# Kernel optimization log

Hardware: AMD Instinct MI355X
Metric: run time of the kernel (lower is better)

Reference implementation:

```python
import jax, jax.numpy as jnp
import numpy as np

B, ZP, ZR, H, MEL, CH, RHY, T = 64, 128, 128, 2048, 130, 12, 3, 32


def _gru(x, h, wih, whh, bih, bhh):
    # torch.nn.GRUCell semantics, gate order (r, z, n)
    gi = x @ wih.T + bih
    gh = h @ whh.T + bhh
    ir, iz, inn = jnp.split(gi, 3, axis=-1)
    hr, hz, hn = jnp.split(gh, 3, axis=-1)
    r = jax.nn.sigmoid(ir + hr)
    u = jax.nn.sigmoid(iz + hz)
    n = jnp.tanh(inn + r * hn)
    return (1.0 - u) * n + u * h


def setup_inputs() -> dict:
    key = jax.random.key(0)
    ks = jax.random.split(key, 13)
    s = 0.02
    rn = lambda k, shp: jax.random.normal(k, shp, dtype=jnp.float32) * s
    return {
        'z1': jax.random.normal(ks[0], (B, ZP), dtype=jnp.float32),
        'z2': jax.random.normal(ks[1], (B, ZR), dtype=jnp.float32),
        'condition': jax.random.uniform(ks[2], (B, T, CH), dtype=jnp.float32),
        'w_ih0': rn(ks[3], (3 * H, ZR + RHY)), 'w_hh0': rn(ks[4], (3 * H, H)),
        'b_ih0': jnp.zeros((3 * H,), jnp.float32), 'b_hh0': jnp.zeros((3 * H,), jnp.float32),
        'w_ih1': rn(ks[5], (3 * H, ZP + MEL + RHY + CH)), 'w_hh1': rn(ks[6], (3 * H, H)),
        'b_ih1': jnp.zeros((3 * H,), jnp.float32), 'b_hh1': jnp.zeros((3 * H,), jnp.float32),
        'w_ih2': rn(ks[7], (3 * H, H)), 'w_hh2': rn(ks[8], (3 * H, H)),
        'b_ih2': jnp.zeros((3 * H,), jnp.float32), 'b_hh2': jnp.zeros((3 * H,), jnp.float32),
        'wi0': rn(ks[9], (H, ZR)), 'bi0': jnp.zeros((H,), jnp.float32),
        'wo0': rn(ks[10], (RHY, H)), 'bo0': jnp.zeros((RHY,), jnp.float32),
        'wi1': rn(ks[11], (H, ZP)), 'bi1': jnp.zeros((H,), jnp.float32),
        'wo1': rn(ks[12], (MEL, H)), 'bo1': jnp.zeros((MEL,), jnp.float32),
    }


def _forward(z1, z2, condition, w_ih0, w_hh0, b_ih0, b_hh0, w_ih1, w_hh1, b_ih1,
             b_hh1, w_ih2, w_hh2, b_ih2, b_hh2, wi0, bi0, wo0, bo0, wi1, bi1, wo1, bo1):
    b = z1.shape[0]

    # --- rhythm decoder (teacher_force=False: argmax one-hot feedback) ---
    def rhy_step(carry, _):
        out, hx = carry
        hx = _gru(jnp.concatenate([out, z2], axis=1), hx, w_ih0, w_hh0, b_ih0, b_hh0)
        lo = jax.nn.log_softmax(hx @ wo0.T + bo0, axis=-1)  # [b, RHY]
        out = jax.nn.one_hot(jnp.argmax(lo, axis=1), RHY, dtype=lo.dtype)
        return (out, hx), lo

    out0 = jnp.zeros((b, RHY), jnp.float32).at[:, -1].set(1.0)
    h0 = jnp.tanh(z2 @ wi0.T + bi0)
    _, rhy = jax.lax.scan(rhy_step, (out0, h0), None, length=T)  # [T, b, RHY]

    # --- final (melody) decoder ---
    def fin_step(carry, xt):
        out, ha, hb = carry
        r_t, c_t, i = xt
        inp = jnp.concatenate([out, r_t, z1, c_t], axis=1)  # [b, MEL+RHY+ZP+CH]
        ha = _gru(inp, ha, w_ih1, w_hh1, b_ih1, b_hh1)
        hb = _gru(ha, jnp.where(i == 0, ha, hb), w_ih2, w_hh2, b_ih2, b_hh2)
        lo = jax.nn.log_softmax(hb @ wo1.T + bo1, axis=-1)  # [b, MEL]
        out = jax.nn.one_hot(jnp.argmax(lo, axis=1), MEL, dtype=lo.dtype)
        return (out, ha, hb), lo

    outm = jnp.zeros((b, MEL), jnp.float32).at[:, -1].set(1.0)
    h1 = jnp.tanh(z1 @ wi1.T + bi1)
    cond_t = jnp.transpose(condition, (1, 0, 2))  # [T, b, CH]
    _, mel = jax.lax.scan(fin_step, (outm, h1, jnp.zeros_like(h1)),
                          (rhy, cond_t, jnp.arange(T)))
    return jnp.transpose(mel, (1, 0, 2))  # [b, T, MEL]


def reference(z1, z2, condition, w_ih0, w_hh0, b_ih0, b_hh0, w_ih1, w_hh1, b_ih1,
              b_hh1, w_ih2, w_hh2, b_ih2, b_hh2, wi0, bi0, wo0, bo0, wi1, bi1, wo1, bo1):
    return _forward(z1, z2, condition, w_ih0, w_hh0, b_ih0, b_hh0, w_ih1, w_hh1,
                    b_ih1, b_hh1, w_ih2, w_hh2, b_ih2, b_hh2, wi0, bi0, wo0, bo0,
                    wi1, bi1, wo1, bo1)
```

## Files before the change

### kernel.cpp

```cpp
#include <hip/hip_runtime.h>
#include <hip/hip_bf16.h>
#include <math.h>

#define Bsz  64
#define Hd   2048
#define G3   6144
#define MELn 130
#define CHn  12
#define RHYn 3
#define Tn   32

__device__ __forceinline__ float sigf(float x) { return 1.0f / (1.0f + expf(-x)); }

__global__ void prep_misc(const float* __restrict__ z1, const float* __restrict__ z2,
                          const float* __restrict__ cond,
                          float* __restrict__ z1t, float* __restrict__ z2t,
                          float* __restrict__ cond_t, int* __restrict__ rhy_idx,
                          int* __restrict__ mel_idx, int* __restrict__ cnts)
{
    int idx = blockIdx.x * 256 + threadIdx.x;
    if (idx < 128 * Bsz) {
        int j = idx >> 6, b = idx & 63;
        z1t[idx] = z1[b * 128 + j];
        z2t[idx] = z2[b * 128 + j];
    }
    if (idx < Tn * CHn * Bsz) {
        int t = idx / (CHn * Bsz);
        int r = idx - t * CHn * Bsz;
        int j = r >> 6, b = r & 63;
        cond_t[idx] = cond[b * (Tn * CHn) + t * CHn + j];
    }
    if (idx < Bsz) { rhy_idx[idx] = RHYn - 1; mel_idx[idx] = MELn - 1; }
    if (idx < 4) cnts[idx] = 0;
}

__global__ __launch_bounds__(256) void init_h_k(
    const float* __restrict__ z1t, const float* __restrict__ z2t,
    const float* __restrict__ wi0, const float* __restrict__ bi0,
    const float* __restrict__ wi1, const float* __restrict__ bi1,
    float* __restrict__ h0_out, float* __restrict__ h1_out)
{
    int lane = threadIdx.x & 63, wave = threadIdx.x >> 6;
    int j = blockIdx.x * 4 + wave;
    int which = blockIdx.y;
    const float* zt = which ? z1t : z2t;
    const float* wi = which ? wi1 : wi0;
    const float* bi = which ? bi1 : bi0;
    float* outh = which ? h1_out : h0_out;
    const float4* w4 = (const float4*)(wi + (size_t)j * 128);
    float acc = 0.f;
#pragma unroll 8
    for (int i = 0; i < 32; i++) {
        float4 w = w4[i];
        int k = i * 4;
        acc = fmaf(zt[(k + 0) * 64 + lane], w.x, acc);
        acc = fmaf(zt[(k + 1) * 64 + lane], w.y, acc);
        acc = fmaf(zt[(k + 2) * 64 + lane], w.z, acc);
        acc = fmaf(zt[(k + 3) * 64 + lane], w.w, acc);
    }
    outh[j * 64 + lane] = tanhf(acc + bi[j]);
}

__global__ __launch_bounds__(256) void gi_const_k(
    const float* __restrict__ z1t, const float* __restrict__ z2t,
    const float* __restrict__ w_ih0, const float* __restrict__ b_ih0,
    const float* __restrict__ w_ih1, const float* __restrict__ b_ih1,
    float* __restrict__ gi0c, float* __restrict__ gi1c)
{
    int lane = threadIdx.x & 63, wave = threadIdx.x >> 6;
    int row = blockIdx.x * 4 + wave;
    int which = blockIdx.y;
    const float* zt; const float* w; float acc; float* dst;
    if (which == 0) { zt = z2t; w = w_ih0 + (size_t)row * 131 + RHYn;          acc = b_ih0[row]; dst = gi0c; }
    else            { zt = z1t; w = w_ih1 + (size_t)row * 273 + (MELn + RHYn); acc = b_ih1[row]; dst = gi1c; }
#pragma unroll 4
    for (int i = 0; i < 128; i++) acc = fmaf(zt[i * 64 + lane], w[i], acc);
    dst[(size_t)row * 64 + lane] = acc;
}

__device__ __forceinline__ void transpose_body(
    const float* __restrict__ in, float* __restrict__ out, int R, int C, int Rout,
    int bx, int by, float* tile)
{
    int c0 = bx * 64, r0 = by * 64;
    int t = threadIdx.x;
    int cl = t & 63, rw = t >> 6;
#pragma unroll
    for (int i = 0; i < 16; ++i) {
        int rl = rw + i * 4;
        int r = r0 + rl, c = c0 + cl;
        float v = (r < R && c < C) ? in[(size_t)r * C + c] : 0.f;
        tile[rl * 65 + cl] = v;
    }
    __syncthreads();
#pragma unroll
    for (int i = 0; i < 16; ++i) {
        int c_loc = rw + i * 4;
        int r_loc = cl;
        int oc = c0 + c_loc, orow = r0 + r_loc;
        if (oc < C && orow < R)
            out[(size_t)oc * Rout + orow] = tile[r_loc * 65 + c_loc];
    }
}

__global__ __launch_bounds__(256) void transpose4_k(
    const float* __restrict__ a, const float* __restrict__ b,
    const float* __restrict__ c, const float* __restrict__ d,
    float* __restrict__ oa, float* __restrict__ ob,
    float* __restrict__ oc, float* __restrict__ od)
{
    __shared__ float tile[64 * 65];
    const float* in; float* out;
    switch (blockIdx.z) {
        case 0: in = a; out = oa; break;
        case 1: in = b; out = ob; break;
        case 2: in = c; out = oc; break;
        default: in = d; out = od; break;
    }
    transpose_body(in, out, G3, Hd, G3, blockIdx.x, blockIdx.y, tile);
}

__global__ __launch_bounds__(256) void transpose1_k(
    const float* __restrict__ in, float* __restrict__ out, int R, int C, int Rout)
{
    __shared__ float tile[64 * 65];
    transpose_body(in, out, R, C, Rout, blockIdx.x, blockIdx.y, tile);
}

__device__ __forceinline__ void mm8_body(
    const float* __restrict__ WT, const float* __restrict__ x,
    float* __restrict__ part, int tile, int slot, float* xs)
{
    int tid = threadIdx.x;
    int rg = tid & 15, bg = tid >> 4;
    int r0 = tile * 128 + rg * 8;
    int b0 = bg * 4;

    float acc[8][4];
#pragma unroll
    for (int i = 0; i < 8; i++)
#pragma unroll
        for (int j = 0; j < 4; j++) acc[i][j] = 0.f;

    for (int ph = 0; ph < 2; ++ph) {
        int kp = slot * 256 + ph * 128;
        __syncthreads();
        {
            const float4* src = (const float4*)(x + (size_t)kp * 64);
            float4* dst = (float4*)xs;
#pragma unroll
            for (int i = 0; i < 8; i++) dst[tid + i * 256] = src[tid + i * 256];
        }
        __syncthreads();
        const float* wp = WT + (size_t)kp * G3 + r0;
#pragma unroll 4
        for (int k = 0; k < 128; ++k) {
            float4 xv = *(const float4*)&xs[k * 64 + b0];
            float w[8];
            *(float4*)&w[0] = *(const float4*)wp;
            *(float4*)&w[4] = *(const float4*)(wp + 4);
            wp += G3;
#pragma unroll
            for (int i = 0; i < 8; i++) {
                acc[i][0] = fmaf(w[i], xv.x, acc[i][0]);
                acc[i][1] = fmaf(w[i], xv.y, acc[i][1]);
                acc[i][2] = fmaf(w[i], xv.z, acc[i][2]);
                acc[i][3] = fmaf(w[i], xv.w, acc[i][3]);
            }
        }
    }

    size_t base = (size_t)slot * 393216 + b0;
    int prow0 = tile * 128 + rg * 8;
#pragma unroll
    for (int i = 0; i < 8; i++)
        *(float4*)&part[base + (size_t)(prow0 + i) * 64] = *(float4*)acc[i];
}

__global__ __launch_bounds__(256) void fusedA_k(
    const float* __restrict__ WT0h, const float* __restrict__ hr, float* __restrict__ partR,
    const float* __restrict__ wo0, const float* __restrict__ bo0,
    float* __restrict__ rlo_prev, int* __restrict__ rhy_idx,
    const float* __restrict__ WT1h, const float* __restrict__ ha, float* __restrict__ partM,
    const float* __restrict__ WTo1, const float* __restrict__ hbPrev,
    float* __restrict__ lpart, const float* __restrict__ bo1,
    float* __restrict__ outp, int tout, int* __restrict__ mel_idx,
    int* __restrict__ cnt, int flags)
{
    __shared__ float smem[8192];
    int flat = blockIdx.x, tid = threadIdx.x;

    if (flat == 0) {
        if (!(flags & 2)) return;
        int lane = tid & 63, wv = tid >> 6;
        const float* hc = hr + wv * 512 * 64;
        const float* w0 = wo0 + wv * 512;
        const float* w1 = wo0 + Hd + wv * 512;
        const float* w2 = wo0 + 2 * Hd + wv * 512;
        float a0 = 0.f, a1 = 0.f, a2 = 0.f;
#pragma unroll 4
        for (int k = 0; k < 512; k++) {
            float hv = hc[k * 64 + lane];
            a0 = fmaf(hv, w0[k], a0);
            a1 = fmaf(hv, w1[k], a1);
            a2 = fmaf(hv, w2[k], a2);
        }
        smem[(0 * 4 + wv) * 64 + lane] = a0;
        smem[(1 * 4 + wv) * 64 + lane] = a1;
        smem[(2 * 4 + wv) * 64 + lane] = a2;
        __syncthreads();
        if (wv == 0) {
            float l0 = smem[0 * 64 + lane] + smem[1 * 64 + lane] + smem[2 * 64 + lane] + smem[3 * 64 + lane] + bo0[0];
            float l1 = smem[4 * 64 + lane] + smem[5 * 64 + lane] + smem[6 * 64 + lane] + smem[7 * 64 + lane] + bo0[1];
            float l2 = smem[8 * 64 + lane] + smem[9 * 64 + lane] + smem[10 * 64 + lane] + smem[11 * 64 + lane] + bo0[2];
            int am; float mx;
            if (l0 >= l1 && l0 >= l2) { am = 0; mx = l0; }
            else if (l1 >= l2)        { am = 1; mx = l1; }
            else                      { am = 2; mx = l2; }
            float s = expf(l0 - mx) + expf(l1 - mx) + expf(l2 - mx);
            float ls = logf(s);
            rlo_prev[lane * 3 + 0] = l0 - mx - ls;
            rlo_prev[lane * 3 + 1] = l1 - mx - ls;
            rlo_prev[lane * 3 + 2] = l2 - mx - ls;
            rhy_idx[lane] = am;
        }
        return;
    }

    if (flat <= 16) {
        if (!(flags & 8)) return;
        int li = flat - 1;
        int ltile = li & 1, lslot = li >> 1;
        int rg = tid & 15, bg = tid >> 4;
        int r0 = ltile * 128 + rg * 8;
        int b0 = bg * 4;
        int k0 = lslot * 256;

        float acc[8][4];
#pragma unroll
        for (int i = 0; i < 8; i++)
#pragma unroll
            for (int j = 0; j < 4; j++) acc[i][j] = 0.f;

        bool fast = (r0 + 7 < MELn);
        for (int ph = 0; ph < 2; ++ph) {
            int kp = k0 + ph * 128;
            __syncthreads();
            {
                const float4* src = (const float4*)(hbPrev + (size_t)kp * 64);
                float4* dst = (float4*)smem;
#pragma unroll
                for (int i = 0; i < 8; i++) dst[tid + i * 256] = src[tid + i * 256];
            }
            __syncthreads();
            if (fast) {
                const float* wp = WTo1 + (size_t)kp * 132 + r0;
#pragma unroll 4
                for (int k = 0; k < 128; ++k) {
                    float4 xv = *(const float4*)&smem[k * 64 + b0];
                    float w[8];
                    *(float4*)&w[0] = *(const float4*)wp;
                    *(float4*)&w[4] = *(const float4*)(wp + 4);
                    wp += 132;
#pragma unroll
                    for (int i = 0; i < 8; i++) {
                        acc[i][0] = fmaf(w[i], xv.x, acc[i][0]);
                        acc[i][1] = fmaf(w[i], xv.y, acc[i][1]);
                        acc[i][2] = fmaf(w[i], xv.z, acc[i][2]);
                        acc[i][3] = fmaf(w[i], xv.w, acc[i][3]);
                    }
                }
            } else {
                for (int k = 0; k < 128; ++k) {
                    float4 xv = *(const float4*)&smem[k * 64 + b0];
                    const float* wrow = WTo1 + (size_t)(k0 + ph * 128 + k) * 132;
                    float w[8];
#pragma unroll
                    for (int i = 0; i < 8; i++) {
                        int rc = r0 + i; if (rc > MELn - 1) rc = MELn - 1;
                        w[i] = wrow[rc];
                    }
#pragma unroll
                    for (int i = 0; i < 8; i++) {
                        acc[i][0] = fmaf(w[i], xv.x, acc[i][0]);
                        acc[i][1] = fmaf(w[i], xv.y, acc[i][1]);
                        acc[i][2] = fmaf(w[i], xv.z, acc[i][2]);
                        acc[i][3] = fmaf(w[i], xv.w, acc[i][3]);
                    }
                }
            }
        }
        size_t base = (size_t)lslot * 8320 + b0;
#pragma unroll
        for (int i = 0; i < 8; i++) {
            int prow = ltile * 128 + rg * 8 + i;
            int pc = prow < MELn ? prow : (MELn - 1);
            *(float4*)&lpart[base + (size_t)pc * 64] = *(float4*)acc[i];
        }

        __shared__ int lastf;
        __threadfence();
        __syncthreads();
        if (tid == 0) lastf = (atomicAdd(cnt, 1) == 15);
        __syncthreads();
        if (!lastf) return;
        __threadfence();

        int b = tid & 63, q = tid >> 6;
        int rLo = q * 33, rHi = rLo + 33; if (rHi > MELn) rHi = MELn;
        float mx = -1e30f; int am = MELn;
        for (int r = rLo; r < rHi; r++) {
            float v = bo1[r];
#pragma unroll
            for (int s = 0; s < 8; s++) v += lpart[s * 8320 + r * 64 + b];
            lpart[r * 64 + b] = v;
            if (v > mx) { mx = v; am = r; }
        }
        float* qmax = smem;
        int*   qam  = (int*)(smem + 256);
        float* qsum = smem + 512;
        qmax[q * 64 + b] = mx; qam[q * 64 + b] = am;
        __syncthreads();
        float gm = qmax[b]; int ga = qam[b];
#pragma unroll
        for (int qq = 1; qq < 4; qq++) {
            float v = qmax[qq * 64 + b];
            if (v > gm) { gm = v; ga = qam[qq * 64 + b]; }
        }
        float ps = 0.f;
        for (int r = rLo; r < rHi; r++) ps += expf(lpart[r * 64 + b] - gm);
        qsum[q * 64 + b] = ps;
        __syncthreads();
        float ls = logf(qsum[b] + qsum[64 + b] + qsum[128 + b] + qsum[192 + b]);
        if (tid < 64) mel_idx[b] = ga;
        for (int r = rLo; r < rHi; r++)
            outp[(size_t)b * Tn * MELn + tout * MELn + r] = lpart[r * 64 + b] - gm - ls;
        __syncthreads();
        if (tid == 0) *cnt = 0;
        return;
    }

    if (flat < 401) {
        if (!(flags & 1)) return;
        int e = flat - 17;
        mm8_body(WT0h, hr, partR, e % 48, e / 48, smem);
        return;
    }
    {
        if (!(flags & 4)) return;
        int e = flat - 401;
        mm8_body(WT1h, ha, partM, e % 48, e / 48, smem);
    }
}

__global__ __launch_bounds__(256) void fusedB_k(
    const float* __restrict__ partR, const float* __restrict__ gi0c,
    const float* __restrict__ w_ih0, const float* __restrict__ b_hh0,
    const float* __restrict__ hr_in, float* __restrict__ hr_out,
    const int* __restrict__ rhy_idx,
    const float* __restrict__ partM, const float* __restrict__ gi1c,
    const float* __restrict__ w_ih1, const float* __restrict__ b_hh1,
    const float* __restrict__ ha_in, float* __restrict__ ha_out,
    const int* __restrict__ mel_idx, const float* __restrict__ rlo,
    const float* __restrict__ cdt, int flags)
{
    __shared__ float red[48 * 68];
    int flat = blockIdx.x, tid = threadIdx.x;
    int wv = tid >> 6, lane = tid & 63;
    int jj = lane >> 4, bq = lane & 15;
    int isMel = (flat >= 512);
    if (isMel) { if (!(flags & 2)) return; }
    else       { if (!(flags & 1)) return; }
    int jbase = (isMel ? flat - 512 : flat) * 4;
    const float* part = isMel ? partM : partR;

    float s0[4], s1[4], s2[4];
#pragma unroll
    for (int q = 0; q < 4; q++) { s0[q] = 0.f; s1[q] = 0.f; s2[q] = 0.f; }
#pragma unroll
    for (int ss = 0; ss < 2; ss++) {
        const float* p = part + (size_t)(wv * 2 + ss) * 393216
                       + (size_t)(jbase + jj) * 64 + bq * 4;
        float4 v0 = *(const float4*)(p);
        float4 v1 = *(const float4*)(p + 2048 * 64);
        float4 v2 = *(const float4*)(p + 4096 * 64);
        s0[0] += v0.x; s0[1] += v0.y; s0[2] += v0.z; s0[3] += v0.w;
        s1[0] += v1.x; s1[1] += v1.y; s1[2] += v1.z; s1[3] += v1.w;
        s2[0] += v2.x; s2[1] += v2.y; s2[2] += v2.z; s2[3] += v2.w;
    }
    int rbase = (wv * 4 + jj) * 3;
    *(float4*)&red[(rbase + 0) * 68 + bq * 4] = make_float4(s0[0], s0[1], s0[2], s0[3]);
    *(float4*)&red[(rbase + 1) * 68 + bq * 4] = make_float4(s1[0], s1[1], s1[2], s1[3]);
    *(float4*)&red[(rbase + 2) * 68 + bq * 4] = make_float4(s2[0], s2[1], s2[2], s2[3]);
    __syncthreads();

    int b = lane, jw = wv;
    int j = jbase + jw;
    float ar = 0.f, az = 0.f, an = 0.f;
#pragma unroll
    for (int ww = 0; ww < 4; ww++) {
        int rb = (ww * 4 + jw) * 3;
        ar += red[(rb + 0) * 68 + b];
        az += red[(rb + 1) * 68 + b];
        an += red[(rb + 2) * 68 + b];
    }

    if (!isMel) {
        int oi = rhy_idx[b];
        float gir = gi0c[j * 64 + b]            + w_ih0[(size_t)j * 131 + oi];
        float giz = gi0c[(j + 2048) * 64 + b]   + w_ih0[(size_t)(j + 2048) * 131 + oi];
        float gin = gi0c[(j + 4096) * 64 + b]   + w_ih0[(size_t)(j + 4096) * 131 + oi];
        float rg = sigf(gir + ar + b_hh0[j]);
        float ug = sigf(giz + az + b_hh0[j + 2048]);
        float ng = tanhf(gin + rg * (an + b_hh0[j + 4096]));
        float hp = hr_in[j * 64 + b];
        hr_out[j * 64 + b] = (1.f - ug) * ng + ug * hp;
    } else {
        int oi = mel_idx[b];
        float r0 = rlo[b * 3 + 0], r1 = rlo[b * 3 + 1], r2 = rlo[b * 3 + 2];
        float cd[12];
#pragma unroll
        for (int q = 0; q < 12; q++) cd[q] = cdt[q * 64 + b];
        float gi[3];
#pragma unroll
        for (int g = 0; g < 3; g++) {
            int row = j + g * 2048;
            const float* wrow = w_ih1 + (size_t)row * 273;
            float v = gi1c[row * 64 + b] + wrow[oi];
            v = fmaf(r0, wrow[130], v);
            v = fmaf(r1, wrow[131], v);
            v = fmaf(r2, wrow[132], v);
#pragma unroll
            for (int q = 0; q < 12; q++) v = fmaf(cd[q], wrow[261 + q], v);
            gi[g] = v;
        }
        float rg = sigf(gi[0] + ar + b_hh1[j]);
        float ug = sigf(gi[1] + az + b_hh1[j + 2048]);
        float ng = tanhf(gi[2] + rg * (an + b_hh1[j + 4096]));
        float hp = ha_in[j * 64 + b];
        ha_out[j * 64 + b] = (1.f - ug) * ng + ug * hp;
    }
}

__global__ __launch_bounds__(256) void mmg2_k(
    const float* __restrict__ WTa, const float* __restrict__ xa,
    const float* __restrict__ WTb, const float* __restrict__ xb,
    float* __restrict__ part)
{
    __shared__ float xs[128 * 64];
    int tid = threadIdx.x;
    int tile = blockIdx.x, slot = blockIdx.y;
    const float* WT; const float* x; int tLoc;
    if (tile < 48) { WT = WTa; x = xa; tLoc = tile; }
    else           { WT = WTb; x = xb; tLoc = tile - 48; }
    int rg = tid & 15, bg = tid >> 4;
    int r0 = tLoc * 128 + rg * 8;
    int b0 = bg * 4;
    int k0 = slot * 512;

    float acc[8][4];
#pragma unroll
    for (int i = 0; i < 8; i++)
#pragma unroll
        for (int j = 0; j < 4; j++) acc[i][j] = 0.f;

    for (int ph = 0; ph < 4; ++ph) {
        int kp = k0 + ph * 128;
        __syncthreads();
        {
            const float4* src = (const float4*)(x + (size_t)kp * 64);
            float4* dst = (float4*)xs;
#pragma unroll
            for (int i = 0; i < 8; i++) dst[tid + i * 256] = src[tid + i * 256];
        }
        __syncthreads();
        const float* wp = WT + (size_t)kp * G3 + r0;
#pragma unroll 4
        for (int k = 0; k < 128; ++k) {
            float4 xv = *(const float4*)&xs[k * 64 + b0];
            float w[8];
            *(float4*)&w[0] = *(const float4*)wp;
            *(float4*)&w[4] = *(const float4*)(wp + 4);
            wp += G3;
#pragma unroll
            for (int i = 0; i < 8; i++) {
                acc[i][0] = fmaf(w[i], xv.x, acc[i][0]);
                acc[i][1] = fmaf(w[i], xv.y, acc[i][1]);
                acc[i][2] = fmaf(w[i], xv.z, acc[i][2]);
                acc[i][3] = fmaf(w[i], xv.w, acc[i][3]);
            }
        }
    }

    size_t base = (size_t)slot * 786432 + b0;
    int prow0 = tile * 128 + rg * 8;
#pragma unroll
    for (int i = 0; i < 8; i++)
        *(float4*)&part[base + (size_t)(prow0 + i) * 64] = *(float4*)acc[i];
}

__global__ __launch_bounds__(256) void mel2_epi(
    const float* __restrict__ part, const float* __restrict__ b_ih,
    const float* __restrict__ b_hh, const float* __restrict__ hb_in,
    float* __restrict__ hb_out)
{
    __shared__ float red[96 * 68];
    int tid = threadIdx.x;
    int wv = tid >> 6, lane = tid & 63;
    int jj = lane >> 4, bq = lane & 15;
    int jbase = blockIdx.x * 4;

    float s[6][4];
    {
        const float* p = part + (size_t)wv * 786432
                       + (size_t)(jbase + jj) * 64 + bq * 4;
#pragma unroll
        for (int g = 0; g < 6; g++) {
            float4 v = *(const float4*)(p + (size_t)g * 2048 * 64);
            s[g][0] = v.x; s[g][1] = v.y; s[g][2] = v.z; s[g][3] = v.w;
        }
    }
    int rbase = (wv * 4 + jj) * 6;
#pragma unroll
    for (int g = 0; g < 6; g++)
        *(float4*)&red[(rbase + g) * 68 + bq * 4] = make_float4(s[g][0], s[g][1], s[g][2], s[g][3]);
    __syncthreads();

    int b = lane, jw = wv;
    int j = jbase + jw;
    float air = 0.f, aiz = 0.f, ain = 0.f, ahr = 0.f, ahz = 0.f, ahn = 0.f;
#pragma unroll
    for (int ww = 0; ww < 4; ww++) {
        int rb = (ww * 4 + jw) * 6;
        air += red[(rb + 0) * 68 + b];
        aiz += red[(rb + 1) * 68 + b];
        ain += red[(rb + 2) * 68 + b];
        ahr += red[(rb + 3) * 68 + b];
        ahz += red[(rb + 4) * 68 + b];
        ahn += red[(rb + 5) * 68 + b];
    }
    float rg = sigf(air + b_ih[j] + ahr + b_hh[j]);
    float ug = sigf(aiz + b_ih[j + 2048] + ahz + b_hh[j + 2048]);
    float ng = tanhf(ain + b_ih[j + 4096] + rg * (ahn + b_hh[j + 4096]));
    float hp = hb_in[j * 64 + b];
    hb_out[j * 64 + b] = (1.f - ug) * ng + ug * hp;
}

__global__ __launch_bounds__(256) void mm2_k(
    const float* __restrict__ WTa, const float* __restrict__ xa,
    const float* __restrict__ WTb, const float* __restrict__ xb,
    float* __restrict__ part, int splitTile, int kc, int nrows, int wstride,
    int partStride)
{
    __shared__ float xs[128 * 64];
    int tid = threadIdx.x;
    int tile = blockIdx.x, slot = blockIdx.y;
    const float* WT; const float* x; int tLoc;
    if (tile < splitTile) { WT = WTa; x = xa; tLoc = tile; }
    else                  { WT = WTb; x = xb; tLoc = tile - splitTile; }
    int rg = tid & 15, bg = tid >> 4;
    int r0 = tLoc * 128 + rg * 8;
    int b0 = bg * 4;
    int k0 = slot * kc;

    float acc[8][4];
#pragma unroll
    for (int i = 0; i < 8; i++)
#pragma unroll
        for (int j = 0; j < 4; j++) acc[i][j] = 0.f;

    bool fast = (r0 + 7 < nrows);
    int nPhase = kc >> 7;
    for (int ph = 0; ph < nPhase; ++ph) {
        int kp = k0 + ph * 128;
        __syncthreads();
        {
            const float4* src = (const float4*)(x + (size_t)kp * 64);
            float4* dst = (float4*)xs;
#pragma unroll
            for (int i = 0; i < 8; i++) dst[tid + i * 256] = src[tid + i * 256];
        }
        __syncthreads();
        if (fast) {
            const float* wp = WT + (size_t)kp * wstride + r0;
#pragma unroll 4
            for (int k = 0; k < 128; ++k) {
                float4 xv = *(const float4*)&xs[k * 64 + b0];
                float w[8];
                *(float4*)&w[0] = *(const float4*)wp;
                *(float4*)&w[4] = *(const float4*)(wp + 4);
                wp += wstride;
#pragma unroll
                for (int i = 0; i < 8; i++) {
                    acc[i][0] = fmaf(w[i], xv.x, acc[i][0]);
                    acc[i][1] = fmaf(w[i], xv.y, acc[i][1]);
                    acc[i][2] = fmaf(w[i], xv.z, acc[i][2]);
                    acc[i][3] = fmaf(w[i], xv.w, acc[i][3]);
                }
            }
        } else {
            for (int k = 0; k < 128; ++k) {
                float4 xv = *(const float4*)&xs[k * 64 + b0];
                const float* wrow = WT + (size_t)(kp + k) * wstride;
                float w[8];
#pragma unroll
                for (int i = 0; i < 8; i++) {
                    int rc = r0 + i; if (rc > nrows - 1) rc = nrows - 1;
                    w[i] = wrow[rc];
                }
#pragma unroll
                for (int i = 0; i < 8; i++) {
                    acc[i][0] = fmaf(w[i], xv.x, acc[i][0]);
                    acc[i][1] = fmaf(w[i], xv.y, acc[i][1]);
                    acc[i][2] = fmaf(w[i], xv.z, acc[i][2]);
                    acc[i][3] = fmaf(w[i], xv.w, acc[i][3]);
                }
            }
        }
    }

    size_t base = (size_t)slot * partStride + b0;
#pragma unroll
    for (int i = 0; i < 8; i++) {
        int prow = tile * 128 + rg * 8 + i;
        int pc = prow < nrows ? prow : (nrows - 1);
        if (tile >= splitTile) pc = prow;
        *(float4*)&part[base + (size_t)pc * 64] = *(float4*)acc[i];
    }
}

__global__ __launch_bounds__(256) void mel_smax(
    const float* __restrict__ part, const float* __restrict__ bo1,
    float* __restrict__ outp, int t, int* __restrict__ mel_idx)
{
    int b = blockIdx.x, tid = threadIdx.x;
    float v = -1e30f;
    if (tid < MELn) {
        v = bo1[tid];
#pragma unroll
        for (int s = 0; s < 16; s++) v += part[s * 8320 + tid * 64 + b];
    }
    __shared__ float smax[256];
    __shared__ int   sidx[256];
    __shared__ float ssum[256];
    smax[tid] = v; sidx[tid] = tid;
    __syncthreads();
    for (int s = 128; s > 0; s >>= 1) {
        if (tid < s) {
            float a = smax[tid], o = smax[tid + s];
            int ai = sidx[tid], oi = sidx[tid + s];
            if (o > a || (o == a && oi < ai)) { smax[tid] = o; sidx[tid] = oi; }
        }
        __syncthreads();
    }
    float mx = smax[0]; int am = sidx[0];
    ssum[tid] = (tid < MELn) ? expf(v - mx) : 0.f;
    __syncthreads();
    for (int s = 128; s > 0; s >>= 1) {
        if (tid < s) ssum[tid] += ssum[tid + s];
        __syncthreads();
    }
    float ls = logf(ssum[0]);
    if (tid < MELn) outp[(size_t)b * Tn * MELn + t * MELn + tid] = v - mx - ls;
    if (tid == 0) mel_idx[b] = am;
}

extern "C" void kernel_launch(void* const* d_in, const int* in_sizes, int n_in,
                              void* d_out, int out_size, void* d_ws, size_t ws_size,
                              hipStream_t stream)
{
    (void)in_sizes; (void)n_in; (void)out_size; (void)ws_size;
    const float* z1    = (const float*)d_in[0];
    const float* z2    = (const float*)d_in[1];
    const float* cond  = (const float*)d_in[2];
    const float* w_ih0 = (const float*)d_in[3];
    const float* w_hh0 = (const float*)d_in[4];
    const float* b_ih0 = (const float*)d_in[5];
    const float* b_hh0 = (const float*)d_in[6];
    const float* w_ih1 = (const float*)d_in[7];
    const float* w_hh1 = (const float*)d_in[8];
    const float* b_ih1 = (const float*)d_in[9];
    const float* b_hh1 = (const float*)d_in[10];
    const float* w_ih2 = (const float*)d_in[11];
    const float* w_hh2 = (const float*)d_in[12];
    const float* b_ih2 = (const float*)d_in[13];
    const float* b_hh2 = (const float*)d_in[14];
    const float* wi0   = (const float*)d_in[15];
    const float* bi0   = (const float*)d_in[16];
    const float* wo0   = (const float*)d_in[17];
    const float* bo0   = (const float*)d_in[18];
    const float* wi1   = (const float*)d_in[19];
    const float* bi1   = (const float*)d_in[20];
    const float* wo1   = (const float*)d_in[21];
    const float* bo1   = (const float*)d_in[22];
    float* outp = (float*)d_out;
    float* ws = (float*)d_ws;

    size_t off = 0;
    float* WT0  = ws + off; off += 12582912;
    float* WT1  = ws + off; off += 12582912;
    float* WTi2 = ws + off; off += 12582912;
    float* WTh2 = ws + off; off += 12582912;
    float* WTo1 = ws + off; off += 270336;
    float* bufR  = ws + off; off += 3145728;
    float* bufMG = ws + off; off += 3145728;
    float* lpart = ws + off; off += 66560;
    float* hR[2] = { ws + off, ws + off + 131072 }; off += 262144;
    float* hA[2] = { ws + off, ws + off + 131072 }; off += 262144;
    float* hB[2] = { ws + off, ws + off + 131072 }; off += 262144;
    float* gi0c   = ws + off; off += 393216;
    float* gi1c   = ws + off; off += 393216;
    float* rlo    = ws + off; off += 6144;
    float* cond_t = ws + off; off += 24576;
    float* z1t    = ws + off; off += 8192;
    float* z2t    = ws + off; off += 8192;
    int* rhy_idx  = (int*)(ws + off); off += 64;
    int* mel_idx  = (int*)(ws + off); off += 64;
    int* cnts     = (int*)(ws + off); off += 64;

    prep_misc<<<96, 256, 0, stream>>>(z1, z2, cond, z1t, z2t, cond_t, rhy_idx, mel_idx, cnts);
    init_h_k<<<dim3(Hd / 4, 2), 256, 0, stream>>>(z1t, z2t, wi0, bi0, wi1, bi1, hR[0], hA[0]);
    gi_const_k<<<dim3(G3 / 4, 2), 256, 0, stream>>>(z1t, z2t, w_ih0, b_ih0, w_ih1, b_ih1, gi0c, gi1c);
    transpose4_k<<<dim3(32, 96, 4), 256, 0, stream>>>(w_hh0, w_hh1, w_ih2, w_hh2,
                                                      WT0, WT1, WTi2, WTh2);
    transpose1_k<<<dim3(32, 3), 256, 0, stream>>>(wo1, WTo1, MELn, Hd, 132);

    for (int u = 0; u <= Tn; u++) {
        int doRhy  = (u < Tn) ? 1 : 0;
        int doRlog = (u >= 1) ? 1 : 0;
        int doMel  = (u >= 1) ? 1 : 0;
        int doMlog = (u >= 2) ? 1 : 0;
        int flagsA = doRhy | (doRlog << 1) | (doMel << 2) | (doMlog << 3);

        const float* hr = hR[u & 1];
        const float* ha_in = (u >= 1) ? hA[(u - 1) & 1] : hA[0];
        const float* hbPrev = (u >= 2) ? hB[(u - 1) & 1] : hB[0];
        float* rloPrev = rlo + (size_t)(u >= 1 ? u - 1 : 0) * 192;

        fusedA_k<<<785, 256, 0, stream>>>(WT0, hr, bufR, wo0, bo0, rloPrev, rhy_idx,
                                          WT1, ha_in, bufMG, WTo1, hbPrev, lpart, bo1,
                                          outp, u - 2, mel_idx, cnts + 0, flagsA);

        fusedB_k<<<1024, 256, 0, stream>>>(bufR, gi0c, w_ih0, b_hh0, hr, hR[(u + 1) & 1],
                                           rhy_idx, bufMG, gi1c, w_ih1, b_hh1,
                                           ha_in, hA[u & 1], mel_idx, rloPrev,
                                           cond_t + (size_t)(u >= 1 ? u - 1 : 0) * (CHn * Bsz),
                                           doRhy | (doMel << 1));

        if (u >= 1) {
            const float* hbop = (u == 1) ? (const float*)hA[u & 1] : (const float*)hB[(u - 1) & 1];
            mmg2_k<<<dim3(96, 4), 256, 0, stream>>>(WTi2, hA[u & 1], WTh2, hbop, bufMG);
            mel2_epi<<<512, 256, 0, stream>>>(bufMG, b_ih2, b_hh2, hbop, hB[u & 1]);
        }
    }

    mm2_k<<<dim3(2, 16), 256, 0, stream>>>(WTo1, hB[0], WTo1, hB[0], bufR,
                                           2, 128, MELn, 132, 8320);
    mel_smax<<<Bsz, 256, 0, stream>>>(bufR, bo1, outp, 31, mel_idx);
}
```

Measured before the change: 5.888 ms.

## Move layer-2 hidden GEMM into fused kernel and vectorize weight transpose

The layer-2 GRU hidden-state GEMM (W_hh2·hb_prev) depends only on the previous step's hb, so it is now computed inside fusedA_k as 192 extra blocks running alongside the other step GEMMs. The separate post-step kernel then only computes the input GEMM (W_ih2·ha), split into 8 K-slots, and the epilogue sums the gi and gh partial sums from separate buffers. This shortens the serial critical path of each timestep by removing half of the dependent GEMM work. Separately, the weight transpose now uses float4 loads and stores. The cost is extra workspace, more blocks in fusedA, and a special case at u==1.

```diff
diff --git a/kernel.cpp b/kernel.cpp
--- a/kernel.cpp
+++ b/kernel.cpp
@@ -78,32 +78,7 @@
     dst[(size_t)row * 64 + lane] = acc;
 }
 
-__device__ __forceinline__ void transpose_body(
-    const float* __restrict__ in, float* __restrict__ out, int R, int C, int Rout,
-    int bx, int by, float* tile)
-{
-    int c0 = bx * 64, r0 = by * 64;
-    int t = threadIdx.x;
-    int cl = t & 63, rw = t >> 6;
-#pragma unroll
-    for (int i = 0; i < 16; ++i) {
-        int rl = rw + i * 4;
-        int r = r0 + rl, c = c0 + cl;
-        float v = (r < R && c < C) ? in[(size_t)r * C + c] : 0.f;
-        tile[rl * 65 + cl] = v;
-    }
-    __syncthreads();
-#pragma unroll
-    for (int i = 0; i < 16; ++i) {
-        int c_loc = rw + i * 4;
-        int r_loc = cl;
-        int oc = c0 + c_loc, orow = r0 + r_loc;
-        if (oc < C && orow < R)
-            out[(size_t)oc * Rout + orow] = tile[r_loc * 65 + c_loc];
-    }
-}
-
-__global__ __launch_bounds__(256) void transpose4_k(
+__global__ __launch_bounds__(256) void transpose4v_k(
     const float* __restrict__ a, const float* __restrict__ b,
     const float* __restrict__ c, const float* __restrict__ d,
     float* __restrict__ oa, float* __restrict__ ob,
@@ -117,19 +92,60 @@
         case 2: in = c; out = oc; break;
         default: in = d; out = od; break;
     }
-    transpose_body(in, out, G3, Hd, G3, blockIdx.x, blockIdx.y, tile);
+    int c0 = blockIdx.x * 64, r0 = blockIdx.y * 64;
+    int t = threadIdx.x;
+    int rq = t & 15, rw = t >> 4;
+#pragma unroll
+    for (int i = 0; i < 4; i++) {
+        int rl = rw + i * 16;
+        float4 v = *(const float4*)&in[(size_t)(r0 + rl) * 2048 + c0 + rq * 4];
+        tile[rl * 65 + rq * 4 + 0] = v.x;
+        tile[rl * 65 + rq * 4 + 1] = v.y;
+        tile[rl * 65 + rq * 4 + 2] = v.z;
+        tile[rl * 65 + rq * 4 + 3] = v.w;
+    }
+    __syncthreads();
+#pragma unroll
+    for (int i = 0; i < 4; i++) {
+        int cl = rw + i * 16;
+        int r4 = rq * 4;
+        float4 w;
+        w.x = tile[(r4 + 0) * 65 + cl];
+        w.y = tile[(r4 + 1) * 65 + cl];
+        w.z = tile[(r4 + 2) * 65 + cl];
+        w.w = tile[(r4 + 3) * 65 + cl];
+        *(float4*)&out[(size_t)(c0 + cl) * G3 + r0 + r4] = w;
+    }
 }
 
 __global__ __launch_bounds__(256) void transpose1_k(
     const float* __restrict__ in, float* __restrict__ out, int R, int C, int Rout)
 {
     __shared__ float tile[64 * 65];
-    transpose_body(in, out, R, C, Rout, blockIdx.x, blockIdx.y, tile);
-}
-
-__device__ __forceinline__ void mm8_body(
+    int c0 = blockIdx.x * 64, r0 = blockIdx.y * 64;
+    int t = threadIdx.x;
+    int cl = t & 63, rw = t >> 6;
+#pragma unroll
+    for (int i = 0; i < 16; ++i) {
+        int rl = rw + i * 4;
+        int r = r0 + rl, c = c0 + cl;
+        float v = (r < R && c < C) ? in[(size_t)r * C + c] : 0.f;
+        tile[rl * 65 + cl] = v;
+    }
+    __syncthreads();
+#pragma unroll
+    for (int i = 0; i < 16; ++i) {
+        int c_loc = rw + i * 4;
+        int r_loc = cl;
+        int oc = c0 + c_loc, orow = r0 + r_loc;
+        if (oc < C && orow < R)
+            out[(size_t)oc * Rout + orow] = tile[r_loc * 65 + c_loc];
+    }
+}
+
+__device__ __forceinline__ void mmP_body(
     const float* __restrict__ WT, const float* __restrict__ x,
-    float* __restrict__ part, int tile, int slot, float* xs)
+    float* __restrict__ partSlot, int tile, int k0, int nPhase, float* xs)
 {
     int tid = threadIdx.x;
     int rg = tid & 15, bg = tid >> 4;
@@ -142,8 +158,8 @@
 #pragma unroll
         for (int j = 0; j < 4; j++) acc[i][j] = 0.f;
 
-    for (int ph = 0; ph < 2; ++ph) {
-        int kp = slot * 256 + ph * 128;
+    for (int ph = 0; ph < nPhase; ++ph) {
+        int kp = k0 + ph * 128;
         __syncthreads();
         {
             const float4* src = (const float4*)(x + (size_t)kp * 64);
@@ -170,11 +186,10 @@
         }
     }
 
-    size_t base = (size_t)slot * 393216 + b0;
     int prow0 = tile * 128 + rg * 8;
 #pragma unroll
     for (int i = 0; i < 8; i++)
-        *(float4*)&part[base + (size_t)(prow0 + i) * 64] = *(float4*)acc[i];
+        *(float4*)&partSlot[(size_t)(prow0 + i) * 64 + b0] = *(float4*)acc[i];
 }
 
 __global__ __launch_bounds__(256) void fusedA_k(
@@ -185,7 +200,8 @@
     const float* __restrict__ WTo1, const float* __restrict__ hbPrev,
     float* __restrict__ lpart, const float* __restrict__ bo1,
     float* __restrict__ outp, int tout, int* __restrict__ mel_idx,
-    int* __restrict__ cnt, int flags)
+    int* __restrict__ cnt,
+    const float* __restrict__ WTh2, float* __restrict__ partGh, int flags)
 {
     __shared__ float smem[8192];
     int flat = blockIdx.x, tid = threadIdx.x;
@@ -273,7 +289,7 @@
             } else {
                 for (int k = 0; k < 128; ++k) {
                     float4 xv = *(const float4*)&smem[k * 64 + b0];
-                    const float* wrow = WTo1 + (size_t)(k0 + ph * 128 + k) * 132;
+                    const float* wrow = WTo1 + (size_t)(kp + k) * 132;
                     float w[8];
 #pragma unroll
                     for (int i = 0; i < 8; i++) {
@@ -343,14 +359,32 @@
     if (flat < 401) {
         if (!(flags & 1)) return;
         int e = flat - 17;
-        mm8_body(WT0h, hr, partR, e % 48, e / 48, smem);
+        int slot = e / 48;
+        mmP_body(WT0h, hr, partR + (size_t)slot * 393216, e % 48, slot * 256, 2, smem);
         return;
     }
-    {
+    if (flat < 785) {
         if (!(flags & 4)) return;
         int e = flat - 401;
-        mm8_body(WT1h, ha, partM, e % 48, e / 48, smem);
-    }
+        int slot = e / 48;
+        mmP_body(WT1h, ha, partM + (size_t)slot * 393216, e % 48, slot * 256, 2, smem);
+        return;
+    }
+    {
+        if (!(flags & 16)) return;
+        int e = flat - 785;
+        int slot = e / 48;
+        mmP_body(WTh2, hbPrev, partGh + (size_t)slot * 393216, e % 48, slot * 512, 4, smem);
+    }
+}
+
+__global__ __launch_bounds__(256) void mmG_k(
+    const float* __restrict__ WT, const float* __restrict__ x,
+    float* __restrict__ part, int kc)
+{
+    __shared__ float xs[8192];
+    int slot = blockIdx.y;
+    mmP_body(WT, x, part + (size_t)slot * 393216, blockIdx.x, slot * kc, kc >> 7, xs);
 }
 
 __global__ __launch_bounds__(256) void fusedB_k(
@@ -442,67 +476,10 @@
     }
 }
 
-__global__ __launch_bounds__(256) void mmg2_k(
-    const float* __restrict__ WTa, const float* __restrict__ xa,
-    const float* __restrict__ WTb, const float* __restrict__ xb,
-    float* __restrict__ part)
-{
-    __shared__ float xs[128 * 64];
-    int tid = threadIdx.x;
-    int tile = blockIdx.x, slot = blockIdx.y;
-    const float* WT; const float* x; int tLoc;
-    if (tile < 48) { WT = WTa; x = xa; tLoc = tile; }
-    else           { WT = WTb; x = xb; tLoc = tile - 48; }
-    int rg = tid & 15, bg = tid >> 4;
-    int r0 = tLoc * 128 + rg * 8;
-    int b0 = bg * 4;
-    int k0 = slot * 512;
-
-    float acc[8][4];
-#pragma unroll
-    for (int i = 0; i < 8; i++)
-#pragma unroll
-        for (int j = 0; j < 4; j++) acc[i][j] = 0.f;
-
-    for (int ph = 0; ph < 4; ++ph) {
-        int kp = k0 + ph * 128;
-        __syncthreads();
-        {
-            const float4* src = (const float4*)(x + (size_t)kp * 64);
-            float4* dst = (float4*)xs;
-#pragma unroll
-            for (int i = 0; i < 8; i++) dst[tid + i * 256] = src[tid + i * 256];
-        }
-        __syncthreads();
-        const float* wp = WT + (size_t)kp * G3 + r0;
-#pragma unroll 4
-        for (int k = 0; k < 128; ++k) {
-            float4 xv = *(const float4*)&xs[k * 64 + b0];
-            float w[8];
-            *(float4*)&w[0] = *(const float4*)wp;
-            *(float4*)&w[4] = *(const float4*)(wp + 4);
-            wp += G3;
-#pragma unroll
-            for (int i = 0; i < 8; i++) {
-                acc[i][0] = fmaf(w[i], xv.x, acc[i][0]);
-                acc[i][1] = fmaf(w[i], xv.y, acc[i][1]);
-                acc[i][2] = fmaf(w[i], xv.z, acc[i][2]);
-                acc[i][3] = fmaf(w[i], xv.w, acc[i][3]);
-            }
-        }
-    }
-
-    size_t base = (size_t)slot * 786432 + b0;
-    int prow0 = tile * 128 + rg * 8;
-#pragma unroll
-    for (int i = 0; i < 8; i++)
-        *(float4*)&part[base + (size_t)(prow0 + i) * 64] = *(float4*)acc[i];
-}
-
 __global__ __launch_bounds__(256) void mel2_epi(
-    const float* __restrict__ part, const float* __restrict__ b_ih,
-    const float* __restrict__ b_hh, const float* __restrict__ hb_in,
-    float* __restrict__ hb_out)
+    const float* __restrict__ gi, const float* __restrict__ gh,
+    const float* __restrict__ b_ih, const float* __restrict__ b_hh,
+    const float* __restrict__ hb_in, float* __restrict__ hb_out)
 {
     __shared__ float red[96 * 68];
     int tid = threadIdx.x;
@@ -511,13 +488,27 @@
     int jbase = blockIdx.x * 4;
 
     float s[6][4];
+#pragma unroll
+    for (int g = 0; g < 6; g++)
+#pragma unroll
+        for (int q = 0; q < 4; q++) s[g][q] = 0.f;
+#pragma unroll
+    for (int ss = 0; ss < 2; ss++) {
+        const float* p = gi + (size_t)(wv * 2 + ss) * 393216
+                       + (size_t)(jbase + jj) * 64 + bq * 4;
+#pragma unroll
+        for (int g = 0; g < 3; g++) {
+            float4 v = *(const float4*)(p + (size_t)g * 2048 * 64);
+            s[g][0] += v.x; s[g][1] += v.y; s[g][2] += v.z; s[g][3] += v.w;
+        }
+    }
     {
-        const float* p = part + (size_t)wv * 786432
+        const float* p = gh + (size_t)wv * 393216
                        + (size_t)(jbase + jj) * 64 + bq * 4;
 #pragma unroll
-        for (int g = 0; g < 6; g++) {
+        for (int g = 0; g < 3; g++) {
             float4 v = *(const float4*)(p + (size_t)g * 2048 * 64);
-            s[g][0] = v.x; s[g][1] = v.y; s[g][2] = v.z; s[g][3] = v.w;
+            s[3 + g][0] = v.x; s[3 + g][1] = v.y; s[3 + g][2] = v.z; s[3 + g][3] = v.w;
         }
     }
     int rbase = (wv * 4 + jj) * 6;
@@ -703,7 +694,8 @@
     float* WTh2 = ws + off; off += 12582912;
     float* WTo1 = ws + off; off += 270336;
     float* bufR  = ws + off; off += 3145728;
-    float* bufMG = ws + off; off += 3145728;
+    float* bufM  = ws + off; off += 3145728;
+    float* bufGh = ws + off; off += 1572864;
     float* lpart = ws + off; off += 66560;
     float* hR[2] = { ws + off, ws + off + 131072 }; off += 262144;
     float* hA[2] = { ws + off, ws + off + 131072 }; off += 262144;
@@ -717,12 +709,13 @@
     int* rhy_idx  = (int*)(ws + off); off += 64;
     int* mel_idx  = (int*)(ws + off); off += 64;
     int* cnts     = (int*)(ws + off); off += 64;
+    float* bufGi = bufR;
 
     prep_misc<<<96, 256, 0, stream>>>(z1, z2, cond, z1t, z2t, cond_t, rhy_idx, mel_idx, cnts);
     init_h_k<<<dim3(Hd / 4, 2), 256, 0, stream>>>(z1t, z2t, wi0, bi0, wi1, bi1, hR[0], hA[0]);
     gi_const_k<<<dim3(G3 / 4, 2), 256, 0, stream>>>(z1t, z2t, w_ih0, b_ih0, w_ih1, b_ih1, gi0c, gi1c);
-    transpose4_k<<<dim3(32, 96, 4), 256, 0, stream>>>(w_hh0, w_hh1, w_ih2, w_hh2,
-                                                      WT0, WT1, WTi2, WTh2);
+    transpose4v_k<<<dim3(32, 96, 4), 256, 0, stream>>>(w_hh0, w_hh1, w_ih2, w_hh2,
+                                                       WT0, WT1, WTi2, WTh2);
     transpose1_k<<<dim3(32, 3), 256, 0, stream>>>(wo1, WTo1, MELn, Hd, 132);
 
     for (int u = 0; u <= Tn; u++) {
@@ -730,27 +723,31 @@
         int doRlog = (u >= 1) ? 1 : 0;
         int doMel  = (u >= 1) ? 1 : 0;
         int doMlog = (u >= 2) ? 1 : 0;
-        int flagsA = doRhy | (doRlog << 1) | (doMel << 2) | (doMlog << 3);
+        int doG2h  = (u >= 2) ? 1 : 0;
+        int flagsA = doRhy | (doRlog << 1) | (doMel << 2) | (doMlog << 3) | (doG2h << 4);
 
         const float* hr = hR[u & 1];
         const float* ha_in = (u >= 1) ? hA[(u - 1) & 1] : hA[0];
         const float* hbPrev = (u >= 2) ? hB[(u - 1) & 1] : hB[0];
         float* rloPrev = rlo + (size_t)(u >= 1 ? u - 1 : 0) * 192;
 
-        fusedA_k<<<785, 256, 0, stream>>>(WT0, hr, bufR, wo0, bo0, rloPrev, rhy_idx,
-                                          WT1, ha_in, bufMG, WTo1, hbPrev, lpart, bo1,
-                                          outp, u - 2, mel_idx, cnts + 0, flagsA);
+        fusedA_k<<<977, 256, 0, stream>>>(WT0, hr, bufR, wo0, bo0, rloPrev, rhy_idx,
+                                          WT1, ha_in, bufM, WTo1, hbPrev, lpart, bo1,
+                                          outp, u - 2, mel_idx, cnts + 0,
+                                          WTh2, bufGh, flagsA);
 
         fusedB_k<<<1024, 256, 0, stream>>>(bufR, gi0c, w_ih0, b_hh0, hr, hR[(u + 1) & 1],
-                                           rhy_idx, bufMG, gi1c, w_ih1, b_hh1,
+                                           rhy_idx, bufM, gi1c, w_ih1, b_hh1,
                                            ha_in, hA[u & 1], mel_idx, rloPrev,
                                            cond_t + (size_t)(u >= 1 ? u - 1 : 0) * (CHn * Bsz),
                                            doRhy | (doMel << 1));
 
         if (u >= 1) {
             const float* hbop = (u == 1) ? (const float*)hA[u & 1] : (const float*)hB[(u - 1) & 1];
-            mmg2_k<<<dim3(96, 4), 256, 0, stream>>>(WTi2, hA[u & 1], WTh2, hbop, bufMG);
-            mel2_epi<<<512, 256, 0, stream>>>(bufMG, b_ih2, b_hh2, hbop, hB[u & 1]);
+            if (u == 1)
+                mmG_k<<<dim3(48, 4), 256, 0, stream>>>(WTh2, hbop, bufGh, 512);
+            mmG_k<<<dim3(48, 8), 256, 0, stream>>>(WTi2, hA[u & 1], bufGi, 256);
+            mel2_epi<<<512, 256, 0, stream>>>(bufGi, bufGh, b_ih2, b_hh2, hbop, hB[u & 1]);
         }
     }
 
```

Measured after the change: 5.774 ms. No clear change (-1.9%).
